# Optimization experiments

Measured on AMD Instinct MI355X. Metric: run time of the kernel, lower is better.

Reference implementation:

```python
import jax, jax.numpy as jnp
import numpy as np

D_MODEL = 256
SEQ_L = 4096
BATCH = 8
H = 3 * D_MODEL   # inner width after 3-branch concat
N_STATE = 32      # complex conjugate pairs -> d_state=64 real
KSIZES = (3, 7, 15)
DILATIONS = (1, 2, 4)


def setup_inputs() -> dict:
    k = jax.random.split(jax.random.key(0), 16)
    d = D_MODEL
    def w(ki, shape, scale):
        return jax.random.normal(ki, shape, jnp.float32) * scale
    inp = {"x": jax.random.normal(k[0], (BATCH, SEQ_L, d), jnp.float32)}
    for i, ksz in enumerate(KSIZES):
        inp[f"conv_w{i}"] = w(k[1 + i], (d, d, ksz), (d * ksz) ** -0.5)
        inp[f"conv_b{i}"] = jnp.zeros((d,), jnp.float32)
    inp["gate_w"] = w(k[4], (H, d), d ** -0.5)
    inp["gate_b"] = jnp.zeros((H,), jnp.float32)
    inp["res_w"] = w(k[5], (H, d), d ** -0.5)
    inp["res_b"] = jnp.zeros((H,), jnp.float32)
    # S4D (diagonal SSM) parameters, d_state=64 -> 32 complex pairs
    inp["log_dt"] = jax.random.uniform(k[6], (H,), jnp.float32, np.log(0.001), np.log(0.1))
    inp["A_re"] = -0.5 * jnp.ones((H, N_STATE), jnp.float32)
    inp["A_im"] = jnp.broadcast_to(np.pi * jnp.arange(N_STATE, dtype=jnp.float32), (H, N_STATE)).copy()
    inp["C_re"] = w(k[7], (H, N_STATE), 0.2)
    inp["C_im"] = w(k[8], (H, N_STATE), 0.2)
    inp["Dskip"] = jax.random.normal(k[9], (H,), jnp.float32)
    inp["ln_gamma"] = jnp.ones((H,), jnp.float32)
    inp["ln_beta"] = jnp.zeros((H,), jnp.float32)
    return inp


def _dil_conv(u, w, b, dil):
    # u: [B, C, L], w: [O, I, K], torch 'same' padding (odd kernels)
    y = jax.lax.conv_general_dilated(
        u, w, window_strides=(1,), padding="SAME", rhs_dilation=(dil,),
        dimension_numbers=("NCH", "OIH", "NCH"))
    return y + b[None, :, None]


def _s4d_apply(u, log_dt, A_re, A_im, C_re, C_im, Dskip):
    # u: [B, H, L]; diagonal SSM long convolution via FFT (ZOH discretization)
    L = u.shape[-1]
    dt = jnp.exp(log_dt)                          # [H]
    A = A_re + 1j * A_im                          # [H, N]
    C = C_re + 1j * C_im                          # [H, N]
    dtA = dt[:, None] * A                         # [H, N]
    C_disc = C * (jnp.exp(dtA) - 1.0) / A         # ZOH input matrix folded into C
    t = jnp.arange(L, dtype=jnp.float32)
    vand = jnp.exp(dtA[:, :, None] * t)           # [H, N, L] Vandermonde
    kern = 2.0 * jnp.real(jnp.einsum("hn,hnl->hl", C_disc, vand))  # [H, L]
    n_fft = 2 * L
    kf = jnp.fft.rfft(kern, n_fft)                # [H, n_fft/2+1]
    uf = jnp.fft.rfft(u, n_fft)                   # [B, H, n_fft/2+1]
    y = jnp.fft.irfft(uf * kf[None], n_fft)[..., :L]
    return y + Dskip[None, :, None] * u


def reference(x, conv_w0, conv_b0, conv_w1, conv_b1, conv_w2, conv_b2,
              gate_w, gate_b, res_w, res_b,
              log_dt, A_re, A_im, C_re, C_im, Dskip, ln_gamma, ln_beta):
    u = jnp.transpose(x, (0, 2, 1))               # [B, d, L]
    convs = [
        _dil_conv(u, conv_w0, conv_b0, DILATIONS[0]),
        _dil_conv(u, conv_w1, conv_b1, DILATIONS[1]),
        _dil_conv(u, conv_w2, conv_b2, DILATIONS[2]),
    ]
    combined = jnp.concatenate(convs, axis=1)     # [B, 3d, L]
    gate = jax.nn.sigmoid(jnp.einsum("bdl,od->bol", u, gate_w) + gate_b[None, :, None])
    gated = combined * gate
    s4_out = _s4d_apply(gated, log_dt, A_re, A_im, C_re, C_im, Dskip)
    resid = jnp.einsum("bdl,od->bol", u, res_w) + res_b[None, :, None]
    out = jnp.transpose(s4_out + resid, (0, 2, 1))  # [B, L, 3d]
    mu = jnp.mean(out, axis=-1, keepdims=True)
    var = jnp.mean((out - mu) ** 2, axis=-1, keepdims=True)
    return (out - mu) * jax.lax.rsqrt(var + 1e-5) * ln_gamma + ln_beta
```

## Files before the change

kernel.cpp:

```cpp
#include <hip/hip_runtime.h>
#include <cstdint>
#include <cstddef>


#define B_ 8
#define L_ 4096
#define D_ 256
#define H_ 768
#define NST 32
#define LC 128
#define NC 32

typedef _Float16 f16;
typedef _Float16 f16x8 __attribute__((ext_vector_type(8)));
typedef _Float16 f16x4 __attribute__((ext_vector_type(4)));
typedef _Float16 f16x2 __attribute__((ext_vector_type(2)));
typedef float f32x4 __attribute__((ext_vector_type(4)));

__device__ __forceinline__ f32x4 mfma16(f16x8 a, f16x8 b, f32x4 c) {
  return __builtin_amdgcn_mfma_f32_16x16x32_f16(a, b, c, 0, 0, 0);
}

#define GLDS16(g, l)                                                              \
  __builtin_amdgcn_global_load_lds((const __attribute__((address_space(1))) void*)(g), \
                                   (__attribute__((address_space(3))) void*)(l), 16, 0, 0)

__global__ __launch_bounds__(256) void prep_all(
    const float* __restrict__ x, const float* __restrict__ gate_w,
    const float* __restrict__ res_w,
    const float* __restrict__ w0, const float* __restrict__ w1, const float* __restrict__ w2,
    f16* __restrict__ xh, f16* __restrict__ Ag, float* __restrict__ zbuf,
    f16* __restrict__ A) {
  int bid = blockIdx.x, tid = threadIdx.x;
  if (bid < 8192) {
    int i = (bid * 256 + tid) * 4;
    float4 v = *(const float4*)(x + i);
    xh[i+0]=(f16)v.x; xh[i+1]=(f16)v.y; xh[i+2]=(f16)v.z; xh[i+3]=(f16)v.w;
  } else if (bid < 8384) {
    int i = ((bid - 8192) * 256 + tid) * 4;
    float4 v = *(const float4*)(gate_w + i);
    Ag[i+0]=(f16)v.x; Ag[i+1]=(f16)v.y; Ag[i+2]=(f16)v.z; Ag[i+3]=(f16)v.w;
  } else if (bid < 8576) {
    int i = ((bid - 8384) * 256 + tid) * 4;
    float4 v = *(const float4*)(res_w + i);
    f16* d = Ag + 768 * 256;
    d[i+0]=(f16)v.x; d[i+1]=(f16)v.y; d[i+2]=(f16)v.z; d[i+3]=(f16)v.w;
  } else if (bid == 8576) {
    zbuf[tid] = 0.f;
  } else {
    int idx = (bid - 8577) * 256 + tid;
    const int n0 = 256 * 256 * 3, n1 = 256 * 256 * 7;
    const float* w; int K, base;
    if (idx < n0) { w = w0; K = 3; base = 0; }
    else if (idx < n0 + n1) { idx -= n0; w = w1; K = 7; base = 256 * 768; }
    else { idx -= n0 + n1; w = w2; K = 15; base = 256 * 768 + 256 * 1792; }
    int o = idx / (256 * K); int r = idx - o * (256 * K); int j = r / K; int t = r - j * K;
    A[base + o * (256 * K) + t * 256 + j] = (f16)w[idx];
  }
}

__global__ __launch_bounds__(256) void s4_all(const float* __restrict__ log_dt,
                                              const float* __restrict__ A_re,
                                              const float* __restrict__ A_im,
                                              const float* __restrict__ C_re,
                                              const float* __restrict__ C_im,
                                              f16* __restrict__ A1, f16* __restrict__ A2,
                                              float* __restrict__ WLc,
                                              float* __restrict__ kT) {
  int bid = blockIdx.x, tid = threadIdx.x;
  if (bid < 96) {
    int idx = bid * 256 + tid;
    int h = idx >> 5, n = idx & 31;
    float dt = expf(log_dt[h]);
    float Ar = A_re[idx], Ai = A_im[idx];
    float ar = dt * Ar, ai = dt * Ai;
    float e = expf(ar), sn, cs; sincosf(ai, &sn, &cs);
    float wr = e * cs, wi = e * sn;
    float den = Ar * Ar + Ai * Ai;
    float Er = wr - 1.f, Ei = wi;
    float Cr = C_re[idx], Ci = C_im[idx];
    float nr = Cr * Er - Ci * Ei, ni = Cr * Ei + Ci * Er;
    float Cdr = (nr * Ar + ni * Ai) / den;
    float Cdi = (ni * Ar - nr * Ai) / den;
    f16* A1r = A1 + ((size_t)h * 64 + 2 * n) * LC;
    f16* A1i = A1 + ((size_t)h * 64 + 2 * n + 1) * LC;
    float pr = 1.f, pi = 0.f;
    for (int j = 0; j < LC; ++j) {
      A1r[LC - 1 - j] = (f16)pr; A1i[LC - 1 - j] = (f16)pi;
      float t0 = pr * wr - pi * wi; pi = pr * wi + pi * wr; pr = t0;
    }
    WLc[idx * 2] = pr; WLc[idx * 2 + 1] = pi;
    float qr = wr, qi = wi;
    for (int t = 0; t < LC; ++t) {
      A2[((size_t)h * LC + t) * 64 + 2 * n]     = (f16)(2.f * (Cdr * qr - Cdi * qi));
      A2[((size_t)h * LC + t) * 64 + 2 * n + 1] = (f16)(-2.f * (Cdr * qi + Cdi * qr));
      float t0 = qr * wr - qi * wi; qi = qr * wi + qi * wr; qr = t0;
    }
  } else {
    int idx = (bid - 96) * 256 + tid;
    int h = idx >> 7, j = idx & 127;
    float dt = expf(log_dt[h]);
    float acc = 0.f;
    for (int n = 0; n < NST; ++n) {
      float Ar = A_re[h * 32 + n], Ai = A_im[h * 32 + n];
      float ar = dt * Ar, ai = dt * Ai;
      float e1 = expf(ar), s1, c1; sincosf(ai, &s1, &c1);
      float wr = e1 * c1, wi = e1 * s1;
      float den = Ar * Ar + Ai * Ai;
      float Er = wr - 1.f, Ei = wi;
      float Cr = C_re[h * 32 + n], Ci = C_im[h * 32 + n];
      float nr = Cr * Er - Ci * Ei, ni = Cr * Ei + Ci * Er;
      float Cdr = (nr * Ar + ni * Ai) / den, Cdi = (ni * Ar - nr * Ai) / den;
      float ej = expf(ar * (float)j), sj, cj; sincosf(ai * (float)j, &sj, &cj);
      acc += 2.f * (Cdr * (ej * cj) - Cdi * (ej * sj));
    }
    kT[idx] = acc;
  }
}

__global__ __launch_bounds__(256) void gemm_gr(
    const f16* __restrict__ xh, const f16* __restrict__ Agr,
    const float* __restrict__ gate_b, const float* __restrict__ res_b,
    f16* __restrict__ gts, f16* __restrict__ res) {
  __shared__ f16 As[128 * 64];
  __shared__ f16 Bs[128 * 64];
  const int mt = blockIdx.y, nt = blockIdx.x;
  const int b = nt >> 5, l0 = (nt & 31) * 128;
  const bool isg = mt < 6;
  const int hbase = (isg ? mt : mt - 6) * 128;
  const f16* Abase = Agr + (size_t)((isg ? 0 : 768) + hbase) * 256;
  const int tid = threadIdx.x;
  const int wid = tid >> 6, lane = tid & 63, l15 = lane & 15, quad = lane >> 4;
  const int wm = (wid & 1) * 64, wn = (wid >> 1) * 64;
  const int srow = (wid << 5) + (lane >> 3);
  const int sperm = ((lane & 7) ^ (lane >> 3)) << 3;
  char* AsL = (char*)As + (wid << 12);
  char* BsL = (char*)Bs + (wid << 12);
  const f16* xrow = xh + (((size_t)b * L_) << 8);

  f32x4 acc[4][4];
#pragma unroll
  for (int i = 0; i < 4; ++i)
#pragma unroll
    for (int j = 0; j < 4; ++j) acc[i][j] = (f32x4){0.f, 0.f, 0.f, 0.f};

  for (int kc = 0; kc < 4; ++kc) {
#pragma unroll
    for (int j = 0; j < 4; ++j) {
      int row = srow + j * 8;
      GLDS16(Abase + (size_t)row * 256 + kc * 64 + sperm, AsL + (j << 10));
      GLDS16(xrow + ((size_t)(l0 + row) << 8) + kc * 64 + sperm, BsL + (j << 10));
    }
    __syncthreads();
#pragma unroll
    for (int k2 = 0; k2 < 2; ++k2) {
      f16x8 af[4], bf[4];
#pragma unroll
      for (int mi = 0; mi < 4; ++mi) {
        int r = wm + mi * 16 + l15;
        af[mi] = *(const f16x8*)(&As[r * 64 + (((k2 * 4 + quad) ^ (r & 7)) << 3)]);
      }
#pragma unroll
      for (int ni = 0; ni < 4; ++ni) {
        int r = wn + ni * 16 + l15;
        bf[ni] = *(const f16x8*)(&Bs[r * 64 + (((k2 * 4 + quad) ^ (r & 7)) << 3)]);
      }
#pragma unroll
      for (int mi = 0; mi < 4; ++mi)
#pragma unroll
        for (int ni = 0; ni < 4; ++ni) acc[mi][ni] = mfma16(af[mi], bf[ni], acc[mi][ni]);
    }
    __syncthreads();
  }

  if (isg) {
#pragma unroll
    for (int mi = 0; mi < 4; ++mi)
#pragma unroll
      for (int ni = 0; ni < 4; ++ni) {
        int hg = hbase + wm + mi * 16 + quad * 4;
        int lg = l0 + wn + ni * 16 + l15;
#pragma unroll
        for (int r = 0; r < 4; ++r) {
          float val = acc[mi][ni][r] + gate_b[hg + r];
          gts[((size_t)(b * H_ + hg + r)) * L_ + lg] = (f16)(1.f / (1.f + expf(-val)));
        }
      }
  } else {
#pragma unroll
    for (int mi = 0; mi < 4; ++mi)
#pragma unroll
      for (int ni = 0; ni < 4; ++ni) {
        int hg = hbase + wm + mi * 16 + quad * 4;
        int lg = l0 + wn + ni * 16 + l15;
#pragma unroll
        for (int r = 0; r < 4; ++r)
          res[((size_t)(b * H_ + hg + r)) * L_ + lg] = (f16)(acc[mi][ni][r] + res_b[hg + r]);
      }
  }
}

__global__ __launch_bounds__(256) void gemm_conv(
    const f16* __restrict__ xh, const f16* __restrict__ Aconv,
    const float* __restrict__ cb0, const float* __restrict__ cb1, const float* __restrict__ cb2,
    const f16* __restrict__ gts, const f16* __restrict__ zbuf,
    f16* __restrict__ v) {
  __shared__ f16 As[128 * 64];
  __shared__ f16 Bs[128 * 64];
  const int mt = blockIdx.y, nt = blockIdx.x;
  const int b = nt >> 5, l0 = (nt & 31) * 128;
  const int ci = 2 - (mt >> 1);
  const int m0 = (mt & 1) * 128;
  const int tid = threadIdx.x;
  const int wid = tid >> 6, lane = tid & 63, l15 = lane & 15, quad = lane >> 4;
  const int wm = (wid & 1) * 64, wn = (wid >> 1) * 64;
  const int srow = (wid << 5) + (lane >> 3);
  const int sperm = ((lane & 7) ^ (lane >> 3)) << 3;
  char* AsL = (char*)As + (wid << 12);
  char* BsL = (char*)Bs + (wid << 12);
  const f16* xrow = xh + (((size_t)b * L_) << 8);

  const f16* Acb; int Krow, taps, dil;
  if (ci == 0)      { Acb = Aconv;                          Krow = 768;  taps = 3;  dil = 1; }
  else if (ci == 1) { Acb = Aconv + 256 * 768;              Krow = 1792; taps = 7;  dil = 2; }
  else              { Acb = Aconv + 256 * 768 + 256 * 1792; Krow = 3840; taps = 15; dil = 4; }

  f32x4 acc[4][4];
#pragma unroll
  for (int i = 0; i < 4; ++i)
#pragma unroll
    for (int j = 0; j < 4; ++j) acc[i][j] = (f32x4){0.f, 0.f, 0.f, 0.f};

  for (int t = 0; t < taps; ++t) {
    const f16* Arows = Acb + (size_t)m0 * Krow + t * 256;
    int boff = (t - (taps - 1) / 2) * dil;
    for (int kc = 0; kc < 4; ++kc) {
#pragma unroll
      for (int j = 0; j < 4; ++j) {
        int row = srow + j * 8;
        GLDS16(Arows + (size_t)row * Krow + kc * 64 + sperm, AsL + (j << 10));
        int gl = l0 + row + boff;
        const f16* gb = xrow + ((size_t)gl << 8) + kc * 64 + sperm;
        if (gl < 0 || gl >= L_) gb = zbuf;
        GLDS16(gb, BsL + (j << 10));
      }
      __syncthreads();
#pragma unroll
      for (int k2 = 0; k2 < 2; ++k2) {
        f16x8 af[4], bf[4];
#pragma unroll
        for (int mi = 0; mi < 4; ++mi) {
          int r = wm + mi * 16 + l15;
          af[mi] = *(const f16x8*)(&As[r * 64 + (((k2 * 4 + quad) ^ (r & 7)) << 3)]);
        }
#pragma unroll
        for (int ni = 0; ni < 4; ++ni) {
          int r = wn + ni * 16 + l15;
          bf[ni] = *(const f16x8*)(&Bs[r * 64 + (((k2 * 4 + quad) ^ (r & 7)) << 3)]);
        }
#pragma unroll
        for (int mi = 0; mi < 4; ++mi)
#pragma unroll
          for (int ni = 0; ni < 4; ++ni) acc[mi][ni] = mfma16(af[mi], bf[ni], acc[mi][ni]);
      }
      __syncthreads();
    }
  }

  const float* cbias = (ci == 0) ? cb0 : (ci == 1 ? cb1 : cb2);
#pragma unroll
  for (int mi = 0; mi < 4; ++mi)
#pragma unroll
    for (int ni = 0; ni < 4; ++ni) {
      int mg = m0 + wm + mi * 16 + quad * 4;
      int lg = l0 + wn + ni * 16 + l15;
#pragma unroll
      for (int r = 0; r < 4; ++r) {
        size_t a = ((size_t)(b * H_ + ci * 256 + mg + r)) * L_ + lg;
        float val = (acc[mi][ni][r] + cbias[mg + r]) * (float)gts[a];
        v[a] = (f16)val;
      }
    }
}

__global__ __launch_bounds__(256) void s1_states(const f16* __restrict__ v,
                                                 const f16* __restrict__ A1,
                                                 const float* __restrict__ WLc,
                                                 f16* __restrict__ Xin) {
  __shared__ f16 A1s[64 * 136];
  __shared__ f16 Vs[128 * 136];
  const int h = blockIdx.y, cb = blockIdx.x;
  const int tid = threadIdx.x;
  {
    int row = tid >> 2, q = tid & 3;
    const f16x8* src = (const f16x8*)(A1 + ((size_t)h * 64 + row) * 128 + q * 32);
    f16x8* dst = (f16x8*)(&A1s[row * 136 + q * 32]);
    dst[0] = src[0]; dst[1] = src[1]; dst[2] = src[2]; dst[3] = src[3];
  }
  {
    int col = tid >> 1, half = tid & 1;
    int cg = cb * 128 + col, b = cg >> 5, c = cg & 31;
    const f16x8* src = (const f16x8*)(v + ((size_t)(b * H_ + h)) * L_ + c * 128 + half * 64);
    f16x8* dst = (f16x8*)(&Vs[col * 136 + half * 64]);
    dst[0] = src[0]; dst[1] = src[1]; dst[2] = src[2]; dst[3] = src[3];
    dst[4] = src[4]; dst[5] = src[5]; dst[6] = src[6]; dst[7] = src[7];
  }
  __syncthreads();
  const int wid = tid >> 6, lane = tid & 63, l15 = lane & 15, quad = lane >> 4;
  const int n0 = wid * 32;
  f32x4 acc[4][2];
#pragma unroll
  for (int i = 0; i < 4; ++i) { acc[i][0] = (f32x4){0,0,0,0}; acc[i][1] = (f32x4){0,0,0,0}; }
#pragma unroll
  for (int bk = 0; bk < 4; ++bk) {
    f16x8 af[4], bf[2];
#pragma unroll
    for (int mi = 0; mi < 4; ++mi)
      af[mi] = *(const f16x8*)(&A1s[(mi * 16 + l15) * 136 + bk * 32 + quad * 8]);
#pragma unroll
    for (int ni = 0; ni < 2; ++ni)
      bf[ni] = *(const f16x8*)(&Vs[(n0 + ni * 16 + l15) * 136 + bk * 32 + quad * 8]);
#pragma unroll
    for (int mi = 0; mi < 4; ++mi)
#pragma unroll
      for (int ni = 0; ni < 2; ++ni) acc[mi][ni] = mfma16(af[mi], bf[ni], acc[mi][ni]);
  }
  __syncthreads();
  float* Xls = (float*)Vs;
#pragma unroll
  for (int mi = 0; mi < 4; ++mi)
#pragma unroll
    for (int ni = 0; ni < 2; ++ni) {
      int col = n0 + ni * 16 + l15;
      *(f32x4*)(&Xls[col * 68 + mi * 16 + quad * 4]) = acc[mi][ni];
    }
  __syncthreads();
  if (tid < 128) {
    int b4 = tid >> 5, n = tid & 31;
    int b = cb * 4 + b4;
    float Wr = WLc[(h * NST + n) * 2], Wi = WLc[(h * NST + n) * 2 + 1];
    float xr = 0.f, xi = 0.f;
    f16* xout = Xin + (((size_t)(b * H_ + h)) * NC) * 64 + 2 * n;
    for (int c = 0; c < NC; ++c) {
      float er = Xls[(b4 * 32 + c) * 68 + 2 * n];
      float ei = Xls[(b4 * 32 + c) * 68 + 2 * n + 1];
      f16x2 o; o[0] = (f16)xr; o[1] = (f16)xi;
      *(f16x2*)(xout + (size_t)c * 64) = o;
      float t = Wr * xr - Wi * xi + er;
      xi = Wr * xi + Wi * xr + ei; xr = t;
    }
  }
}

__global__ __launch_bounds__(256) void s3_output(const f16* __restrict__ v,
                                                 const f16* __restrict__ A2g,
                                                 const f16* __restrict__ res,
                                                 const float* __restrict__ kT,
                                                 const f16* __restrict__ Xin,
                                                 const float* __restrict__ Dskip,
                                                 f16* __restrict__ y4) {
  __shared__ f16 Ts[128 * 136];
  __shared__ f16 Vs[64 * 136];
  __shared__ float kTs[128];
  f16* A2s = Ts;
  f16* Xs = Ts + 128 * 72;
  const int h = blockIdx.y, cb = blockIdx.x;
  const int tid = threadIdx.x;
  if (tid < 128) kTs[tid] = kT[h * 128 + tid];
  {
    int col = tid >> 2, q = tid & 3;
    int cg = cb * 64 + col, b = cg >> 5, c = cg & 31;
    const f16x8* src = (const f16x8*)(v + ((size_t)(b * H_ + h)) * L_ + c * 128 + q * 32);
    f16x8* dst = (f16x8*)(&Vs[col * 136 + q * 32]);
    dst[0] = src[0]; dst[1] = src[1]; dst[2] = src[2]; dst[3] = src[3];
  }
  __syncthreads();
  {
    int tau = tid >> 1, h64 = (tid & 1) * 64;
#pragma unroll
    for (int jv = 0; jv < 8; ++jv) {
      int s0 = h64 + jv * 8;
      f16x8 w;
#pragma unroll
      for (int e = 0; e < 8; ++e) {
        int s = s0 + e;
        w[e] = (f16)((s <= tau) ? kTs[tau - s] : 0.f);
      }
      *(f16x8*)(&Ts[tau * 136 + s0]) = w;
    }
  }
  __syncthreads();
  const int wid = tid >> 6, lane = tid & 63, l15 = lane & 15, quad = lane >> 4;
  const int wm = (wid & 1) * 64, wn = (wid >> 1) * 32;
  f32x4 acc[4][2];
#pragma unroll
  for (int i = 0; i < 4; ++i) { acc[i][0] = (f32x4){0,0,0,0}; acc[i][1] = (f32x4){0,0,0,0}; }
#pragma unroll
  for (int bk = 0; bk < 4; ++bk) {
    f16x8 af[4], bf[2];
#pragma unroll
    for (int mi = 0; mi < 4; ++mi)
      af[mi] = *(const f16x8*)(&Ts[(wm + mi * 16 + l15) * 136 + bk * 32 + quad * 8]);
#pragma unroll
    for (int ni = 0; ni < 2; ++ni)
      bf[ni] = *(const f16x8*)(&Vs[(wn + ni * 16 + l15) * 136 + bk * 32 + quad * 8]);
#pragma unroll
    for (int mi = 0; mi < 4; ++mi)
#pragma unroll
      for (int ni = 0; ni < 2; ++ni) acc[mi][ni] = mfma16(af[mi], bf[ni], acc[mi][ni]);
  }
  __syncthreads();
  {
    int row = tid >> 1, half = tid & 1;
    const f16x8* src = (const f16x8*)(A2g + ((size_t)h * 128 + row) * 64 + half * 32);
    f16x8* dst = (f16x8*)(&A2s[row * 72 + half * 32]);
    dst[0] = src[0]; dst[1] = src[1]; dst[2] = src[2]; dst[3] = src[3];
  }
  {
    int col = tid >> 2, part = tid & 3;
    int cg = cb * 64 + col, b = cg >> 5, c = cg & 31;
    const f16x8* src = (const f16x8*)(Xin + (((size_t)(b * H_ + h)) * NC + c) * 64 + part * 16);
    f16x8* dst = (f16x8*)(&Xs[col * 72 + part * 16]);
    dst[0] = src[0]; dst[1] = src[1];
  }
  __syncthreads();
#pragma unroll
  for (int bk = 0; bk < 2; ++bk) {
    f16x8 af[4], bf[2];
#pragma unroll
    for (int mi = 0; mi < 4; ++mi)
      af[mi] = *(const f16x8*)(&A2s[(wm + mi * 16 + l15) * 72 + bk * 32 + quad * 8]);
#pragma unroll
    for (int ni = 0; ni < 2; ++ni)
      bf[ni] = *(const f16x8*)(&Xs[(wn + ni * 16 + l15) * 72 + bk * 32 + quad * 8]);
#pragma unroll
    for (int mi = 0; mi < 4; ++mi)
#pragma unroll
      for (int ni = 0; ni < 2; ++ni) acc[mi][ni] = mfma16(af[mi], bf[ni], acc[mi][ni]);
  }
  float Dh = Dskip[h];
#pragma unroll
  for (int mi = 0; mi < 4; ++mi)
#pragma unroll
    for (int ni = 0; ni < 2; ++ni) {
      int col = wn + ni * 16 + l15;
      int cg = cb * 64 + col, b = cg >> 5, c = cg & 31;
      int tau0 = wm + mi * 16 + quad * 4;
      size_t lbase = ((size_t)(b * H_ + h)) * L_ + c * 128 + tau0;
      const f16* rp = res + lbase;
      f16x4 o;
#pragma unroll
      for (int r = 0; r < 4; ++r)
        o[r] = (f16)(acc[mi][ni][r] + Dh * (float)Vs[col * 136 + tau0 + r] + (float)rp[r]);
      *(f16x4*)(y4 + lbase) = o;
    }
}

__global__ __launch_bounds__(256) void layernorm_t(const f16* __restrict__ y4,
                                                   const float* __restrict__ gamma,
                                                   const float* __restrict__ beta,
                                                   float* __restrict__ out) {
  __shared__ f16 Ys[768 * 72];
  __shared__ float psum[256], psq[256], mu[64], rs[64];
  const int b = blockIdx.y, l0 = blockIdx.x * 64;
  const int tid = threadIdx.x;
  {
    int r8 = tid >> 3, c = tid & 7;
    for (int it = 0; it < 24; ++it) {
      int hh = it * 32 + r8;
      f16x8 x = *(const f16x8*)(y4 + ((size_t)(b * H_ + hh)) * L_ + l0 + c * 8);
      *(f16x8*)(&Ys[hh * 72 + c * 8]) = x;
    }
  }
  __syncthreads();
  {
    int l = tid & 63, hg = tid >> 6;
    float s = 0.f, s2 = 0.f;
    for (int k = 0; k < 192; ++k) {
      float val = (float)Ys[(hg * 192 + k) * 72 + l];
      s += val; s2 += val * val;
    }
    psum[hg * 64 + l] = s; psq[hg * 64 + l] = s2;
  }
  __syncthreads();
  if (tid < 64) {
    float S = 0.f, S2 = 0.f;
    for (int g = 0; g < 4; ++g) { S += psum[g * 64 + tid]; S2 += psq[g * 64 + tid]; }
    float m = S / 768.f;
    float var = S2 / 768.f - m * m;
    mu[tid] = m; rs[tid] = rsqrtf(var + 1e-5f);
  }
  __syncthreads();
  float g0 = gamma[tid], g1 = gamma[256 + tid], g2 = gamma[512 + tid];
  float be0 = beta[tid], be1 = beta[256 + tid], be2 = beta[512 + tid];
  for (int lv = 0; lv < 8; ++lv) {
    f16x8 y0 = *(const f16x8*)(&Ys[(size_t)tid * 72 + lv * 8]);
    f16x8 y1 = *(const f16x8*)(&Ys[(size_t)(256 + tid) * 72 + lv * 8]);
    f16x8 y2 = *(const f16x8*)(&Ys[(size_t)(512 + tid) * 72 + lv * 8]);
#pragma unroll
    for (int e = 0; e < 8; ++e) {
      int ll = lv * 8 + e;
      float m = mu[ll], r = rs[ll];
      size_t ob = ((size_t)b * L_ + l0 + ll) * H_;
      out[ob + tid]       = ((float)y0[e] - m) * r * g0 + be0;
      out[ob + 256 + tid] = ((float)y1[e] - m) * r * g1 + be1;
      out[ob + 512 + tid] = ((float)y2[e] - m) * r * g2 + be2;
    }
  }
}

extern "C" void kernel_launch(void* const* d_in, const int* in_sizes, int n_in,
                              void* d_out, int out_size, void* d_ws, size_t ws_size,
                              hipStream_t stream) {
  const float* x      = (const float*)d_in[0];
  const float* cw0    = (const float*)d_in[1];
  const float* cb0    = (const float*)d_in[2];
  const float* cw1    = (const float*)d_in[3];
  const float* cb1    = (const float*)d_in[4];
  const float* cw2    = (const float*)d_in[5];
  const float* cb2    = (const float*)d_in[6];
  const float* gate_w = (const float*)d_in[7];
  const float* gate_b = (const float*)d_in[8];
  const float* res_w  = (const float*)d_in[9];
  const float* res_b  = (const float*)d_in[10];
  const float* log_dt = (const float*)d_in[11];
  const float* A_re   = (const float*)d_in[12];
  const float* A_im   = (const float*)d_in[13];
  const float* C_re   = (const float*)d_in[14];
  const float* C_im   = (const float*)d_in[15];
  const float* Dskip  = (const float*)d_in[16];
  const float* ln_g   = (const float*)d_in[17];
  const float* ln_b   = (const float*)d_in[18];
  float* out = (float*)d_out;

  char* ws = (char*)d_ws;
  f16*   xh   = (f16*)(ws + 0);
  f16*   Ac   = (f16*)(ws + 16777216);
  f16*   Ag   = (f16*)(ws + 20054016);
  f16*   zbuf = (f16*)(ws + 20840448);
  f16*   vb   = (f16*)(ws + 20841472);
  f16*   resb = (f16*)(ws + 71173120);
  f16*   gts  = (f16*)(ws + 121504768);
  f16*   A1   = (f16*)(ws + 171836416);
  f16*   A2   = (f16*)(ws + 184419328);
  float* kT   = (float*)(ws + 197002240);
  float* WLc  = (float*)(ws + 197395456);
  f16*   Xin  = (f16*)(ws + 197592064);
  f16*   y4   = (f16*)(ws + 222757888);

  prep_all<<<14977, 256, 0, stream>>>(x, gate_w, res_w, cw0, cw1, cw2,
                                      xh, Ag, (float*)zbuf, Ac);
  s4_all<<<480, 256, 0, stream>>>(log_dt, A_re, A_im, C_re, C_im, A1, A2, WLc, kT);

  gemm_gr<<<dim3(256, 12), 256, 0, stream>>>(xh, Ag, gate_b, res_b, gts, resb);
  gemm_conv<<<dim3(256, 6), 256, 0, stream>>>(xh, Ac, cb0, cb1, cb2, gts, zbuf, vb);

  s1_states<<<dim3(2, 768), 256, 0, stream>>>(vb, A1, WLc, Xin);
  s3_output<<<dim3(4, 768), 256, 0, stream>>>(vb, A2, resb, kT, Xin, Dskip, y4);

  layernorm_t<<<dim3(64, 8), 256, 0, stream>>>(y4, ln_g, ln_b, out);
}
```

Measured before the change: 454.0 us.

## Rewrite conv GEMM as 256x256 tile, 8-wave, double-buffered pipelined kernel

Replaces the 128x128 single-buffered conv GEMM with a 256x256-tile kernel of 512 threads (8 waves). It double-buffers A/B tiles in 128KB of LDS and interleaves async global-to-LDS staging of the next k-step with MFMA quadrants, using explicit barriers, waitcnt and setprio. The intent is to hide global load latency and raise reuse per loaded byte. The risk is lower occupancy and fewer blocks (384), which could leave CUs underused, plus fragile manual vmcnt accounting.

After: 458.9 us. No clear change (+1.1%).

```diff
diff --git a/kernel.cpp b/kernel.cpp
--- a/kernel.cpp
+++ b/kernel.cpp
@@ -200,87 +200,158 @@
   }
 }
 
-__global__ __launch_bounds__(256) void gemm_conv(
+__global__ __launch_bounds__(512, 2) void gemm_conv8(
     const f16* __restrict__ xh, const f16* __restrict__ Aconv,
     const float* __restrict__ cb0, const float* __restrict__ cb1, const float* __restrict__ cb2,
     const f16* __restrict__ gts, const f16* __restrict__ zbuf,
     f16* __restrict__ v) {
-  __shared__ f16 As[128 * 64];
-  __shared__ f16 Bs[128 * 64];
-  const int mt = blockIdx.y, nt = blockIdx.x;
-  const int b = nt >> 5, l0 = (nt & 31) * 128;
-  const int ci = 2 - (mt >> 1);
-  const int m0 = (mt & 1) * 128;
+  __shared__ f16 lds[65536];
+  f16* A0 = lds;
+  f16* B0 = lds + 16384;
+  f16* A1 = lds + 32768;
+  f16* B1 = lds + 49152;
+
+  const int nt = blockIdx.x;
+  const int b = nt >> 4, l0 = (nt & 15) * 256;
+  const int ci = 2 - blockIdx.y;
   const int tid = threadIdx.x;
   const int wid = tid >> 6, lane = tid & 63, l15 = lane & 15, quad = lane >> 4;
-  const int wm = (wid & 1) * 64, wn = (wid >> 1) * 64;
-  const int srow = (wid << 5) + (lane >> 3);
-  const int sperm = ((lane & 7) ^ (lane >> 3)) << 3;
-  char* AsL = (char*)As + (wid << 12);
-  char* BsL = (char*)Bs + (wid << 12);
+  const int wr = wid >> 2, wc = wid & 3;
+  const int r0 = tid >> 3;
+  const int cswz = ((tid & 7) ^ ((tid >> 3) & 7)) << 3;
+  const int rsw = lane & 7;
   const f16* xrow = xh + (((size_t)b * L_) << 8);
 
   const f16* Acb; int Krow, taps, dil;
   if (ci == 0)      { Acb = Aconv;                          Krow = 768;  taps = 3;  dil = 1; }
   else if (ci == 1) { Acb = Aconv + 256 * 768;              Krow = 1792; taps = 7;  dil = 2; }
   else              { Acb = Aconv + 256 * 768 + 256 * 1792; Krow = 3840; taps = 15; dil = 4; }
-
-  f32x4 acc[4][4];
-#pragma unroll
-  for (int i = 0; i < 4; ++i)
+  const int KS = taps * 4;
+
+  f32x4 acc[8][4];
+#pragma unroll
+  for (int i = 0; i < 8; ++i)
 #pragma unroll
     for (int j = 0; j < 4; ++j) acc[i][j] = (f32x4){0.f, 0.f, 0.f, 0.f};
-
-  for (int t = 0; t < taps; ++t) {
-    const f16* Arows = Acb + (size_t)m0 * Krow + t * 256;
+  f16x8 af[4][2], blo[2][2], bhi[2][2];
+
+  auto stageA = [&](int kst, int h, f16* Ad) {
+    int t = kst >> 2, jb = (kst & 3) << 6;
+    const f16* s0 = Acb + (size_t)(h * 128 + r0) * Krow + t * 256 + jb + cswz;
+    GLDS16(s0, Ad + h * 8192 + wid * 512);
+    GLDS16(s0 + (size_t)64 * Krow, Ad + h * 8192 + 4096 + wid * 512);
+  };
+  auto stageB = [&](int kst, int h, f16* Bd) {
+    int t = kst >> 2, jb = (kst & 3) << 6;
     int boff = (t - (taps - 1) / 2) * dil;
-    for (int kc = 0; kc < 4; ++kc) {
-#pragma unroll
-      for (int j = 0; j < 4; ++j) {
-        int row = srow + j * 8;
-        GLDS16(Arows + (size_t)row * Krow + kc * 64 + sperm, AsL + (j << 10));
-        int gl = l0 + row + boff;
-        const f16* gb = xrow + ((size_t)gl << 8) + kc * 64 + sperm;
-        if (gl < 0 || gl >= L_) gb = zbuf;
-        GLDS16(gb, BsL + (j << 10));
-      }
-      __syncthreads();
-#pragma unroll
-      for (int k2 = 0; k2 < 2; ++k2) {
-        f16x8 af[4], bf[4];
-#pragma unroll
-        for (int mi = 0; mi < 4; ++mi) {
-          int r = wm + mi * 16 + l15;
-          af[mi] = *(const f16x8*)(&As[r * 64 + (((k2 * 4 + quad) ^ (r & 7)) << 3)]);
+    int gl0 = l0 + h * 128 + r0 + boff;
+    const f16* s0 = (gl0 < 0 || gl0 >= L_) ? (zbuf + cswz)
+                    : xrow + ((size_t)gl0 << 8) + jb + cswz;
+    GLDS16(s0, Bd + h * 8192 + wid * 512);
+    int gl1 = gl0 + 64;
+    const f16* s1 = (gl1 < 0 || gl1 >= L_) ? (zbuf + cswz)
+                    : xrow + ((size_t)gl1 << 8) + jb + cswz;
+    GLDS16(s1, Bd + h * 8192 + 4096 + wid * 512);
+  };
+  auto loadA = [&](const f16* Ab, int MH) {
+#pragma unroll
+    for (int mi = 0; mi < 4; ++mi) {
+      int r = MH * 128 + wr * 64 + mi * 16 + l15;
+#pragma unroll
+      for (int k2 = 0; k2 < 2; ++k2)
+        af[mi][k2] = *(const f16x8*)(Ab + r * 64 + (((k2 * 4 + quad) ^ rsw) << 3));
+    }
+  };
+  auto loadB = [&](const f16* Bb, int NH, f16x8 (&bf)[2][2]) {
+#pragma unroll
+    for (int ni = 0; ni < 2; ++ni) {
+      int r = NH * 128 + wc * 32 + ni * 16 + l15;
+#pragma unroll
+      for (int k2 = 0; k2 < 2; ++k2)
+        bf[ni][k2] = *(const f16x8*)(Bb + r * 64 + (((k2 * 4 + quad) ^ rsw) << 3));
+    }
+  };
+  auto quadMM = [&](int MH, int NH, f16x8 (&bf)[2][2]) {
+#pragma unroll
+    for (int k2 = 0; k2 < 2; ++k2)
+#pragma unroll
+      for (int mi = 0; mi < 4; ++mi)
+#pragma unroll
+        for (int ni = 0; ni < 2; ++ni)
+          acc[MH * 4 + mi][NH * 2 + ni] =
+              mfma16(af[mi][k2], bf[ni][k2], acc[MH * 4 + mi][NH * 2 + ni]);
+  };
+
+  auto kstep = [&](int kst, f16* Ab, f16* Bb, f16* AbN, f16* BbN) {
+    loadA(Ab, 0); loadB(Bb, 0, blo);
+    if (kst + 1 < KS) stageB(kst + 1, 0, BbN);
+    __builtin_amdgcn_s_barrier();
+    asm volatile("s_waitcnt lgkmcnt(0)" ::: "memory");
+    __builtin_amdgcn_s_setprio(1);
+    quadMM(0, 0, blo);
+    __builtin_amdgcn_s_setprio(0);
+    __builtin_amdgcn_s_barrier();
+    loadB(Bb, 1, bhi);
+    if (kst + 1 < KS) stageA(kst + 1, 1, AbN);
+    __builtin_amdgcn_s_barrier();
+    asm volatile("s_waitcnt lgkmcnt(0)" ::: "memory");
+    __builtin_amdgcn_s_setprio(1);
+    quadMM(0, 1, bhi);
+    __builtin_amdgcn_s_setprio(0);
+    __builtin_amdgcn_s_barrier();
+    loadA(Ab, 1);
+    if (kst + 2 < KS) stageA(kst + 2, 0, Ab);
+    __builtin_amdgcn_s_barrier();
+    asm volatile("s_waitcnt lgkmcnt(0)" ::: "memory");
+    __builtin_amdgcn_s_setprio(1);
+    quadMM(1, 1, bhi);
+    __builtin_amdgcn_s_setprio(0);
+    __builtin_amdgcn_s_barrier();
+    if (kst + 2 < KS) stageB(kst + 2, 1, Bb);
+    __builtin_amdgcn_s_barrier();
+    asm volatile("s_waitcnt lgkmcnt(0)" ::: "memory");
+    __builtin_amdgcn_s_setprio(1);
+    quadMM(1, 0, blo);
+    __builtin_amdgcn_s_setprio(0);
+    if (kst + 2 < KS) asm volatile("s_waitcnt vmcnt(4)" ::: "memory");
+    else              asm volatile("s_waitcnt vmcnt(0)" ::: "memory");
+    __builtin_amdgcn_s_barrier();
+  };
+
+  stageA(0, 0, A0);
+  stageB(0, 1, B0);
+  stageB(0, 0, B0);
+  stageA(0, 1, A0);
+  stageA(1, 0, A1);
+  stageB(1, 1, B1);
+  asm volatile("s_waitcnt vmcnt(4)" ::: "memory");
+  __builtin_amdgcn_s_barrier();
+
+#pragma unroll 1
+  for (int k = 0; k < KS; k += 2) {
+    kstep(k,     A0, B0, A1, B1);
+    kstep(k + 1, A1, B1, A0, B0);
+  }
+
+  const float* cbias = (ci == 0) ? cb0 : (ci == 1 ? cb1 : cb2);
+#pragma unroll
+  for (int mh = 0; mh < 2; ++mh)
+#pragma unroll
+    for (int mi = 0; mi < 4; ++mi)
+#pragma unroll
+      for (int nh = 0; nh < 2; ++nh)
+#pragma unroll
+        for (int ni = 0; ni < 2; ++ni) {
+          int mg = mh * 128 + wr * 64 + mi * 16 + quad * 4;
+          int lg = l0 + nh * 128 + wc * 32 + ni * 16 + l15;
+          f32x4 a4 = acc[mh * 4 + mi][nh * 2 + ni];
+#pragma unroll
+          for (int r = 0; r < 4; ++r) {
+            size_t a = ((size_t)(b * H_ + ci * 256 + mg + r)) * L_ + lg;
+            float val = (a4[r] + cbias[mg + r]) * (float)gts[a];
+            v[a] = (f16)val;
+          }
         }
-#pragma unroll
-        for (int ni = 0; ni < 4; ++ni) {
-          int r = wn + ni * 16 + l15;
-          bf[ni] = *(const f16x8*)(&Bs[r * 64 + (((k2 * 4 + quad) ^ (r & 7)) << 3)]);
-        }
-#pragma unroll
-        for (int mi = 0; mi < 4; ++mi)
-#pragma unroll
-          for (int ni = 0; ni < 4; ++ni) acc[mi][ni] = mfma16(af[mi], bf[ni], acc[mi][ni]);
-      }
-      __syncthreads();
-    }
-  }
-
-  const float* cbias = (ci == 0) ? cb0 : (ci == 1 ? cb1 : cb2);
-#pragma unroll
-  for (int mi = 0; mi < 4; ++mi)
-#pragma unroll
-    for (int ni = 0; ni < 4; ++ni) {
-      int mg = m0 + wm + mi * 16 + quad * 4;
-      int lg = l0 + wn + ni * 16 + l15;
-#pragma unroll
-      for (int r = 0; r < 4; ++r) {
-        size_t a = ((size_t)(b * H_ + ci * 256 + mg + r)) * L_ + lg;
-        float val = (acc[mi][ni][r] + cbias[mg + r]) * (float)gts[a];
-        v[a] = (f16)val;
-      }
-    }
 }
 
 __global__ __launch_bounds__(256) void s1_states(const f16* __restrict__ v,
@@ -553,7 +624,7 @@
   s4_all<<<480, 256, 0, stream>>>(log_dt, A_re, A_im, C_re, C_im, A1, A2, WLc, kT);
 
   gemm_gr<<<dim3(256, 12), 256, 0, stream>>>(xh, Ag, gate_b, res_b, gts, resb);
-  gemm_conv<<<dim3(256, 6), 256, 0, stream>>>(xh, Ac, cb0, cb1, cb2, gts, zbuf, vb);
+  gemm_conv8<<<dim3(128, 3), 512, 0, stream>>>(xh, Ac, cb0, cb1, cb2, gts, zbuf, vb);
 
   s1_states<<<dim3(2, 768), 256, 0, stream>>>(vb, A1, WLc, Xin);
   s3_output<<<dim3(4, 768), 256, 0, stream>>>(vb, A2, resb, kT, Xin, Dskip, y4);
```
